# Kernel tuning notes

Hardware: AMD Instinct MI355X
Metric: run time of the kernel (lower is better)

Reference implementation:

```python
import jax, jax.numpy as jnp
import numpy as np

M, K, N = 32, 4096, 12288


def setup_inputs() -> dict:
    key = jax.random.key(0)
    k1, k2, k3, k4 = jax.random.split(key, 4)
    x = jax.random.normal(k1, (M, K), dtype=jnp.float32)
    # uint8-valued packed weight (stored as int32 for harness compatibility, values in [0,256))
    weight_u8 = jax.random.randint(k2, (K, N), 0, 256, dtype=jnp.int32)
    # per-output-channel fp16 scale and zero-point
    scale = (jax.random.uniform(k3, (N,), dtype=jnp.float32) * 0.01 + 1e-3).astype(jnp.float16)
    zero = (jax.random.uniform(k4, (N,), dtype=jnp.float32) * 255.0).astype(jnp.float16)
    return {"x": x, "weight_u8": weight_u8, "scale": scale, "zero": zero}


def reference(x, weight_u8, scale, zero):
    # QuantMatmulCustom: dequantize uint8 weight with per-channel fp16 scale/zero, then matmul.
    # w_deq[k, n] = (w_u8[k, n] - zero[n]) * scale[n]
    w_deq = (weight_u8.astype(jnp.float32) - zero.astype(jnp.float32)[None, :]) * scale.astype(jnp.float32)[None, :]
    # [M, K] @ [K, N] -> [M, N]
    return jnp.einsum('mk,kn->mn', x, w_deq)
```

## Files before the change

### kernel.cpp

```cpp
#include <hip/hip_runtime.h>

#define M_DIM 32
#define K_DIM 4096
#define N_DIM 12288
#define SPLITK 8
#define KPER  (K_DIM / SPLITK)
#define NT    (KPER / 32)
#define BLK   512
#define NPB   128

using bf16x8 = __attribute__((ext_vector_type(8))) short;
using f32x4  = __attribute__((ext_vector_type(4))) float;

typedef __attribute__((address_space(1))) const void GASV;
typedef __attribute__((address_space(3))) void LASV;

__device__ __forceinline__ short to_bf16(float f) {
    unsigned u = __float_as_uint(f);
    u += 0x7FFFu + ((u >> 16) & 1u);
    return (short)(u >> 16);
}

__device__ __forceinline__ bf16x8 pack_b(const int (&wv)[8]) {
    union { unsigned u[4]; bf16x8 v; } r;
    #pragma unroll
    for (int p = 0; p < 4; ++p) {
        unsigned a = __float_as_uint((float)wv[2 * p]);
        unsigned b = __float_as_uint((float)wv[2 * p + 1]);
        r.u[p] = __builtin_amdgcn_perm(b, a, 0x07060302);
    }
    return r.v;
}

__global__ __launch_bounds__(256) void qmm_prep(const float* __restrict__ x,
                                                short* __restrict__ frag,
                                                float* __restrict__ rowsum,
                                                float* __restrict__ out) {
    const int tid = threadIdx.x;
    const int bid = blockIdx.x;

    ((float4*)out)[bid * 256 + tid] = make_float4(0.f, 0.f, 0.f, 0.f);
    if (bid >= 32) return;
    const int b = bid;

    __shared__ float red[256];
    const float4* xr = (const float4*)(x + (size_t)b * K_DIM);
    float s = 0.f;
    #pragma unroll
    for (int i = 0; i < K_DIM / 4 / 256; ++i) {
        float4 v = xr[tid + 256 * i];
        s += v.x + v.y + v.z + v.w;
    }
    red[tid] = s;
    __syncthreads();
    #pragma unroll
    for (int off = 128; off > 0; off >>= 1) {
        if (tid < off) red[tid] += red[tid + off];
        __syncthreads();
    }
    if (tid == 0) rowsum[b] = red[0];

    #pragma unroll
    for (int i = 0; i < 2; ++i) {
        const int s2   = i * 256 + tid;
        const int kt   = 4 * b + (s2 >> 7);
        const int h    = (s2 >> 6) & 1;
        const int lane = s2 & 63;
        const int g    = lane >> 4;
        const int g0   = g & 1;
        const int m    = 16 * h + (lane & 15);
        const float* xp = x + (size_t)m * K_DIM + kt * 32 + 8 * g;
        float p0 = xp[0], p1 = xp[1], p2 = xp[2], p3 = xp[3];
        float p4 = xp[4], p5 = xp[5], p6 = xp[6], p7 = xp[7];
        bf16x8 v;
        v[0] = to_bf16(g0 ? p1 : p0);  v[1] = to_bf16(g0 ? p0 : p1);
        v[2] = to_bf16(g0 ? p3 : p2);  v[3] = to_bf16(g0 ? p2 : p3);
        v[4] = to_bf16(g0 ? p5 : p4);  v[5] = to_bf16(g0 ? p4 : p5);
        v[6] = to_bf16(g0 ? p7 : p6);  v[7] = to_bf16(g0 ? p6 : p7);
        *(bf16x8*)&frag[(size_t)((kt * 2 + h) * 64 + lane) * 8] = v;
    }
}

__global__ __launch_bounds__(BLK, 4) void qmm_main(const short* __restrict__ frag,
                                                   const int* __restrict__ w,
                                                   const float* __restrict__ rowsum,
                                                   const float* __restrict__ scale,
                                                   const float* __restrict__ zero,
                                                   float* __restrict__ out) {
    __shared__ int lds_b[8 * 2 * 512];

    const int tid  = threadIdx.x;
    const int lane = tid & 63;
    const int g    = lane >> 4;
    const int g0   = g & 1;
    const int c    = lane & 15;
    const int wid  = tid >> 6;
    const int k0   = blockIdx.y * KPER;
    const int n0w  = blockIdx.x * NPB + wid * 16;

    const int* gsrc[2];
    #pragma unroll
    for (int q = 0; q < 2; ++q)
        gsrc[q] = w + (size_t)(k0 + 16 * q + (lane >> 2)) * N_DIM + n0w + 4 * (lane & 3);

    int* const wbase = &lds_b[wid * 1024];

    const int vb = 4 * (128 * g + 4 * (c >> 2) + (c & 3));
    const int be = vb + 64 * g0;
    const int bo = vb + 64 * (1 - g0);

    const short* asrc = frag + ((size_t)(blockIdx.y * NT) * 1024 + lane * 8);

    f32x4 acc0 = {0.f, 0.f, 0.f, 0.f};
    f32x4 acc1 = {0.f, 0.f, 0.f, 0.f};
    bf16x8 aA0, aA1, aB0, aB1;

#define ISSUE(T) do {                                                            \
    __builtin_amdgcn_sched_barrier(0);                                           \
    __builtin_amdgcn_global_load_lds((GASV*)(gsrc[0] + (size_t)(32 * (T)) * N_DIM), \
        (LASV*)(wbase + ((T) & 1) * 512),       16, 0, 0);                       \
    __builtin_amdgcn_global_load_lds((GASV*)(gsrc[1] + (size_t)(32 * (T)) * N_DIM), \
        (LASV*)(wbase + ((T) & 1) * 512 + 256), 16, 0, 0);                       \
    if ((T) & 1) { aB0 = *(const bf16x8*)(asrc + (T) * 1024);                    \
                   aB1 = *(const bf16x8*)(asrc + (T) * 1024 + 512); }            \
    else         { aA0 = *(const bf16x8*)(asrc + (T) * 1024);                    \
                   aA1 = *(const bf16x8*)(asrc + (T) * 1024 + 512); }            \
    __builtin_amdgcn_sched_barrier(0);                                           \
} while (0)

#define WAITV(N) do { asm volatile("s_waitcnt vmcnt(" #N ")" ::: "memory");      \
    __builtin_amdgcn_sched_barrier(0); } while (0)

#define COMP(T) do {                                                             \
    char* pb = (char*)wbase + ((T) & 1) * 2048;                                  \
    int wv[8];                                                                   \
    wv[0] = *(int*)(pb + be);        wv[1] = *(int*)(pb + bo);                   \
    wv[2] = *(int*)(pb + be + 128);  wv[3] = *(int*)(pb + bo + 128);             \
    wv[4] = *(int*)(pb + be + 256);  wv[5] = *(int*)(pb + bo + 256);             \
    wv[6] = *(int*)(pb + be + 384);  wv[7] = *(int*)(pb + bo + 384);             \
    bf16x8 bfv = pack_b(wv);                                                     \
    acc0 = __builtin_amdgcn_mfma_f32_16x16x32_bf16(((T) & 1) ? aB0 : aA0, bfv, acc0, 0, 0, 0); \
    acc1 = __builtin_amdgcn_mfma_f32_16x16x32_bf16(((T) & 1) ? aB1 : aA1, bfv, acc1, 0, 0, 0); \
} while (0)

    ISSUE(0); ISSUE(1);
    WAITV(4); COMP(0);  ISSUE(2);
    WAITV(4); COMP(1);  ISSUE(3);
    WAITV(4); COMP(2);  ISSUE(4);
    WAITV(4); COMP(3);  ISSUE(5);
    WAITV(4); COMP(4);  ISSUE(6);
    WAITV(4); COMP(5);  ISSUE(7);
    WAITV(4); COMP(6);  ISSUE(8);
    WAITV(4); COMP(7);  ISSUE(9);
    WAITV(4); COMP(8);  ISSUE(10);
    WAITV(4); COMP(9);  ISSUE(11);
    WAITV(4); COMP(10); ISSUE(12);
    WAITV(4); COMP(11); ISSUE(13);
    WAITV(4); COMP(12); ISSUE(14);
    WAITV(4); COMP(13); ISSUE(15);
    WAITV(4); COMP(14);
    WAITV(0); COMP(15);

#undef ISSUE
#undef WAITV
#undef COMP

    const float sc = scale[n0w + c];
    float corr0[4] = {0.f, 0.f, 0.f, 0.f}, corr1[4] = {0.f, 0.f, 0.f, 0.f};
    if (blockIdx.y == 0) {
        const float zp = zero[n0w + c];
        #pragma unroll
        for (int i = 0; i < 4; ++i) {
            const int r = 4 * (lane >> 4) + i;
            corr0[i] = zp * rowsum[r];
            corr1[i] = zp * rowsum[16 + r];
        }
    }
    #pragma unroll
    for (int i = 0; i < 4; ++i) {
        const int r = 4 * (lane >> 4) + i;
        atomicAdd(&out[(size_t)r * N_DIM + n0w + c],        sc * (acc0[i] - corr0[i]));
        atomicAdd(&out[(size_t)(16 + r) * N_DIM + n0w + c], sc * (acc1[i] - corr1[i]));
    }
}

__global__ __launch_bounds__(256) void qmm_zero_fb(float* __restrict__ out) {
    int i = blockIdx.x * 256 + threadIdx.x;
    ((float4*)out)[i] = make_float4(0.f, 0.f, 0.f, 0.f);
}
__global__ __launch_bounds__(256) void qmm_main_fb(const float* __restrict__ x,
                                                   const int* __restrict__ w,
                                                   float* __restrict__ out) {
    const int n  = blockIdx.x * 256 + threadIdx.x;
    const int k0 = blockIdx.y * 256;
    float acc[M_DIM];
    #pragma unroll
    for (int m = 0; m < M_DIM; ++m) acc[m] = 0.f;
    const int* wp = w + (size_t)k0 * N_DIM + n;
    for (int kk = 0; kk < 256; kk += 4) {
        const float w0 = (float)wp[(size_t)(kk + 0) * N_DIM];
        const float w1 = (float)wp[(size_t)(kk + 1) * N_DIM];
        const float w2 = (float)wp[(size_t)(kk + 2) * N_DIM];
        const float w3 = (float)wp[(size_t)(kk + 3) * N_DIM];
        #pragma unroll
        for (int m = 0; m < M_DIM; ++m) {
            const float4 xv = *(const float4*)(x + (size_t)m * K_DIM + k0 + kk);
            acc[m] = fmaf(xv.x, w0, fmaf(xv.y, w1, fmaf(xv.z, w2, fmaf(xv.w, w3, acc[m]))));
        }
    }
    #pragma unroll
    for (int m = 0; m < M_DIM; ++m)
        atomicAdd(&out[(size_t)m * N_DIM + n], acc[m]);
}
__global__ __launch_bounds__(256) void qmm_scale_fb(const float* __restrict__ x,
                                                    const float* __restrict__ scale,
                                                    const float* __restrict__ zero,
                                                    float* __restrict__ out) {
    const int m = blockIdx.y;
    __shared__ float red[256];
    float s = 0.f;
    for (int k = threadIdx.x; k < K_DIM; k += 256)
        s += x[(size_t)m * K_DIM + k];
    red[threadIdx.x] = s;
    __syncthreads();
    #pragma unroll
    for (int off = 128; off > 0; off >>= 1) {
        if (threadIdx.x < off) red[threadIdx.x] += red[threadIdx.x + off];
        __syncthreads();
    }
    const float rowsum = red[0];
    const int n = blockIdx.x * 256 + threadIdx.x;
    const float v = out[(size_t)m * N_DIM + n];
    out[(size_t)m * N_DIM + n] = scale[n] * (v - zero[n] * rowsum);
}

extern "C" void kernel_launch(void* const* d_in, const int* in_sizes, int n_in,
                              void* d_out, int out_size, void* d_ws, size_t ws_size,
                              hipStream_t stream) {
    const float* x     = (const float*)d_in[0];
    const int*   w     = (const int*)d_in[1];
    const float* scale = (const float*)d_in[2];
    const float* zero  = (const float*)d_in[3];
    float* out = (float*)d_out;

    const size_t frag_sz = (size_t)128 * 2 * 64 * 8 * sizeof(short);
    short* fragp  = (short*)d_ws;
    float* rowsum = (float*)((char*)d_ws + frag_sz);

    if (ws_size >= frag_sz + 256) {
        qmm_prep<<<dim3(M_DIM * N_DIM / 4 / 256), dim3(256), 0, stream>>>(x, fragp, rowsum, out);
        qmm_main<<<dim3(N_DIM / NPB, SPLITK),     dim3(BLK), 0, stream>>>(fragp, w, rowsum, scale, zero, out);
    } else {
        qmm_zero_fb <<<dim3(M_DIM * N_DIM / 4 / 256), dim3(256), 0, stream>>>(out);
        qmm_main_fb <<<dim3(N_DIM / 256, 16),         dim3(256), 0, stream>>>(x, w, out);
        qmm_scale_fb<<<dim3(N_DIM / 256, M_DIM),      dim3(256), 0, stream>>>(x, scale, zero, out);
    }
}
```

Measured before the change: 43.17 us.

## Share swizzled block-wide LDS weight tiles with barrier-synchronized double buffering

The weight staging moves from per-wave private LDS slices to one block-wide tile. Each wave cooperatively loads rows through an XOR-swizzled global-to-LDS mapping and reads its B fragments with a matching swizzled stride-128 pattern, aiming to cut LDS bank conflicts and simplify fragment reads. The A-fragment preparation drops the even/odd element permutation, since the new B layout no longer needs it. The explicit per-wave vmcnt waits are replaced by a __syncthreads per k-step, which adds block-wide barriers and may shorten the effective prefetch depth.

Result: no change. 43.05 us (-0.3%).

```diff
diff --git a/kernel.cpp b/kernel.cpp
--- a/kernel.cpp
+++ b/kernel.cpp
@@ -67,16 +67,11 @@
         const int h    = (s2 >> 6) & 1;
         const int lane = s2 & 63;
         const int g    = lane >> 4;
-        const int g0   = g & 1;
         const int m    = 16 * h + (lane & 15);
         const float* xp = x + (size_t)m * K_DIM + kt * 32 + 8 * g;
-        float p0 = xp[0], p1 = xp[1], p2 = xp[2], p3 = xp[3];
-        float p4 = xp[4], p5 = xp[5], p6 = xp[6], p7 = xp[7];
         bf16x8 v;
-        v[0] = to_bf16(g0 ? p1 : p0);  v[1] = to_bf16(g0 ? p0 : p1);
-        v[2] = to_bf16(g0 ? p3 : p2);  v[3] = to_bf16(g0 ? p2 : p3);
-        v[4] = to_bf16(g0 ? p5 : p4);  v[5] = to_bf16(g0 ? p4 : p5);
-        v[6] = to_bf16(g0 ? p7 : p6);  v[7] = to_bf16(g0 ? p6 : p7);
+        #pragma unroll
+        for (int j = 0; j < 8; ++j) v[j] = to_bf16(xp[j]);
         *(bf16x8*)&frag[(size_t)((kt * 2 + h) * 64 + lane) * 8] = v;
     }
 }
@@ -87,27 +82,30 @@
                                                    const float* __restrict__ scale,
                                                    const float* __restrict__ zero,
                                                    float* __restrict__ out) {
-    __shared__ int lds_b[8 * 2 * 512];
+    __shared__ int lds_b[2 * 32 * 128];
 
     const int tid  = threadIdx.x;
     const int lane = tid & 63;
     const int g    = lane >> 4;
-    const int g0   = g & 1;
     const int c    = lane & 15;
     const int wid  = tid >> 6;
     const int k0   = blockIdx.y * KPER;
-    const int n0w  = blockIdx.x * NPB + wid * 16;
-
-    const int* gsrc[2];
-    #pragma unroll
-    for (int q = 0; q < 2; ++q)
-        gsrc[q] = w + (size_t)(k0 + 16 * q + (lane >> 2)) * N_DIM + n0w + 4 * (lane & 3);
-
-    int* const wbase = &lds_b[wid * 1024];
-
-    const int vb = 4 * (128 * g + 4 * (c >> 2) + (c & 3));
-    const int be = vb + 64 * g0;
-    const int bo = vb + 64 * (1 - g0);
+    const int n0   = blockIdx.x * NPB;
+    const int n0w  = n0 + wid * 16;
+
+    const int* gs[2];
+    #pragma unroll
+    for (int q = 0; q < 2; ++q) {
+        const int rl = 4 * wid + 2 * q + (lane >> 5);
+        const int gg = (rl >> 3) & 3;
+        const int sw = gg | ((gg & 1) << 2);
+        gs[q] = w + (size_t)(k0 + rl) * N_DIM + n0 + 4 * ((lane & 31) ^ sw);
+    }
+    int* const ld0 = &lds_b[(wid * 2 + 0) * 256];
+    int* const ld1 = &lds_b[(wid * 2 + 1) * 256];
+
+    const int prd = (wid * 16 + c) ^ (g << 2) ^ ((g & 1) << 4);
+    const int* const bq = lds_b + g * 8 * 128 + prd;
 
     const short* asrc = frag + ((size_t)(blockIdx.y * NT) * 1024 + lane * 8);
 
@@ -115,55 +113,45 @@
     f32x4 acc1 = {0.f, 0.f, 0.f, 0.f};
     bf16x8 aA0, aA1, aB0, aB1;
 
-#define ISSUE(T) do {                                                            \
-    __builtin_amdgcn_sched_barrier(0);                                           \
-    __builtin_amdgcn_global_load_lds((GASV*)(gsrc[0] + (size_t)(32 * (T)) * N_DIM), \
-        (LASV*)(wbase + ((T) & 1) * 512),       16, 0, 0);                       \
-    __builtin_amdgcn_global_load_lds((GASV*)(gsrc[1] + (size_t)(32 * (T)) * N_DIM), \
-        (LASV*)(wbase + ((T) & 1) * 512 + 256), 16, 0, 0);                       \
-    if ((T) & 1) { aB0 = *(const bf16x8*)(asrc + (T) * 1024);                    \
-                   aB1 = *(const bf16x8*)(asrc + (T) * 1024 + 512); }            \
-    else         { aA0 = *(const bf16x8*)(asrc + (T) * 1024);                    \
-                   aA1 = *(const bf16x8*)(asrc + (T) * 1024 + 512); }            \
-    __builtin_amdgcn_sched_barrier(0);                                           \
-} while (0)
-
-#define WAITV(N) do { asm volatile("s_waitcnt vmcnt(" #N ")" ::: "memory");      \
-    __builtin_amdgcn_sched_barrier(0); } while (0)
+#define STAGE(T) do { if ((T) < NT) {                                            \
+    __builtin_amdgcn_global_load_lds((GASV*)(gs[0] + (size_t)(32 * (T)) * N_DIM), \
+        (LASV*)(ld0 + ((T) & 1) * 4096), 16, 0, 0);                              \
+    __builtin_amdgcn_global_load_lds((GASV*)(gs[1] + (size_t)(32 * (T)) * N_DIM), \
+        (LASV*)(ld1 + ((T) & 1) * 4096), 16, 0, 0);                              \
+} } while (0)
+
+#define LOADA(T) do { if ((T) < NT) {                                            \
+    if ((T) & 1) { aB0 = *(const bf16x8*)(asrc + (size_t)(T) * 1024);            \
+                   aB1 = *(const bf16x8*)(asrc + (size_t)(T) * 1024 + 512); }    \
+    else         { aA0 = *(const bf16x8*)(asrc + (size_t)(T) * 1024);            \
+                   aA1 = *(const bf16x8*)(asrc + (size_t)(T) * 1024 + 512); }    \
+} } while (0)
 
 #define COMP(T) do {                                                             \
-    char* pb = (char*)wbase + ((T) & 1) * 2048;                                  \
+    const int* bp = bq + ((T) & 1) * 4096;                                       \
     int wv[8];                                                                   \
-    wv[0] = *(int*)(pb + be);        wv[1] = *(int*)(pb + bo);                   \
-    wv[2] = *(int*)(pb + be + 128);  wv[3] = *(int*)(pb + bo + 128);             \
-    wv[4] = *(int*)(pb + be + 256);  wv[5] = *(int*)(pb + bo + 256);             \
-    wv[6] = *(int*)(pb + be + 384);  wv[7] = *(int*)(pb + bo + 384);             \
+    _Pragma("unroll")                                                            \
+    for (int j = 0; j < 8; ++j) wv[j] = bp[j * 128];                             \
     bf16x8 bfv = pack_b(wv);                                                     \
     acc0 = __builtin_amdgcn_mfma_f32_16x16x32_bf16(((T) & 1) ? aB0 : aA0, bfv, acc0, 0, 0, 0); \
     acc1 = __builtin_amdgcn_mfma_f32_16x16x32_bf16(((T) & 1) ? aB1 : aA1, bfv, acc1, 0, 0, 0); \
 } while (0)
 
-    ISSUE(0); ISSUE(1);
-    WAITV(4); COMP(0);  ISSUE(2);
-    WAITV(4); COMP(1);  ISSUE(3);
-    WAITV(4); COMP(2);  ISSUE(4);
-    WAITV(4); COMP(3);  ISSUE(5);
-    WAITV(4); COMP(4);  ISSUE(6);
-    WAITV(4); COMP(5);  ISSUE(7);
-    WAITV(4); COMP(6);  ISSUE(8);
-    WAITV(4); COMP(7);  ISSUE(9);
-    WAITV(4); COMP(8);  ISSUE(10);
-    WAITV(4); COMP(9);  ISSUE(11);
-    WAITV(4); COMP(10); ISSUE(12);
-    WAITV(4); COMP(11); ISSUE(13);
-    WAITV(4); COMP(12); ISSUE(14);
-    WAITV(4); COMP(13); ISSUE(15);
-    WAITV(4); COMP(14);
-    WAITV(0); COMP(15);
-
-#undef ISSUE
-#undef WAITV
+#define ITER(T) do { COMP(T); LOADA((T) + 1); __syncthreads(); STAGE((T) + 2); } while (0)
+
+    STAGE(0); STAGE(1); LOADA(0);
+    __syncthreads();
+
+    ITER(0);  ITER(1);  ITER(2);  ITER(3);
+    ITER(4);  ITER(5);  ITER(6);  ITER(7);
+    ITER(8);  ITER(9);  ITER(10); ITER(11);
+    ITER(12); ITER(13); ITER(14);
+    COMP(15);
+
+#undef STAGE
+#undef LOADA
 #undef COMP
+#undef ITER
 
     const float sc = scale[n0w + c];
     float corr0[4] = {0.f, 0.f, 0.f, 0.f}, corr1[4] = {0.f, 0.f, 0.f, 0.f};
```
